# Optimization experiments

Measured on AMD Instinct MI355X. Metric: run time of the kernel, lower is better.

The kernel has to match this reference:

```python
import jax, jax.numpy as jnp
import numpy as np

L, H, P = 32768, 256, 256
DT_MIN, DT_MAX = 0.001, 0.1


def setup_inputs() -> dict:
    key = jax.random.key(0)
    ks = jax.random.split(key, 7)
    signal = jax.random.normal(ks[0], (L, H), jnp.float32)
    # stable HiPPO-like init: negative real part, random imaginary part
    lam_re = -(0.1 + 0.4 * jax.random.uniform(ks[1], (P,), jnp.float32))
    lam_im = jax.random.normal(ks[2], (P,), jnp.float32)
    Lambda_ri = jnp.stack([lam_re, lam_im], axis=-1)            # (P, 2)
    B_ri = jax.random.normal(ks[3], (P, H, 2), jnp.float32) / np.float32(np.sqrt(H))
    C_ri = jax.random.normal(ks[4], (H, P, 2), jnp.float32) / np.float32(np.sqrt(P))
    D = jax.random.uniform(ks[5], (H,), jnp.float32)
    log_step = jnp.log(DT_MIN + (DT_MAX - DT_MIN) * jax.random.uniform(ks[6], (P,), jnp.float32))
    return {"signal": signal, "Lambda_ri": Lambda_ri, "B_ri": B_ri,
            "C_ri": C_ri, "D": D, "log_step": log_step}


def reference(signal, Lambda_ri, B_ri, C_ri, D, log_step):
    # --- get_BC_tilde (bcInit='dense'): B stored real (P,H,2) -> complex ---
    Lambda = jax.lax.complex(Lambda_ri[..., 0], Lambda_ri[..., 1])   # (P,)
    B_tilde = jax.lax.complex(B_ri[..., 0], B_ri[..., 1])            # (P, H)
    C_tilde = jax.lax.complex(C_ri[..., 0], C_ri[..., 1])            # (H, P)

    # --- discretize_zoh ---
    step = jnp.exp(log_step)                                          # (P,) step_scale = 1.0
    Lambda_bar = jnp.exp(Lambda * step)                               # (P,) complex
    B_bar = ((Lambda_bar - 1.0) / Lambda)[:, None] * B_tilde          # (P, H) complex

    # --- apply_ssm: Bu_elements = vmap(u -> B_bar @ u) over time ---
    Bu = signal.astype(Lambda_bar.dtype) @ B_bar.T                    # (L, P) complex
    Lam = jnp.broadcast_to(Lambda_bar, Bu.shape)                      # (L, P)

    def binop(qi, qj):
        A_i, Bu_i = qi
        A_j, Bu_j = qj
        return (A_j * A_i, Bu_j + A_j * Bu_i)

    _, xs = jax.lax.associative_scan(binop, (Lam, Bu), axis=0)        # (L, P)

    # y = Re(C_tilde @ x) + D * u, vectorized over time
    y = jnp.real(xs @ C_tilde.T) + D * signal                         # (L, H)
    return y
```

## Files before the change

### kernel.cpp

```cpp
#include <hip/hip_runtime.h>
#include <math.h>

constexpr int L = 32768;
constexpr int H = 256;
constexpr int P = 256;
constexpr int T = 64;
constexpr int NC = L / T;
constexpr int N1 = 2 * P;
constexpr int LDA = 40;
constexpr int LDEP = 130;

typedef __attribute__((ext_vector_type(8))) short short8;
typedef __attribute__((ext_vector_type(4))) float f32x4;

__device__ __forceinline__ unsigned f2bf(float f) {
  unsigned u = __float_as_uint(f);
  return (u + 0x7FFFu + ((u >> 16) & 1u)) >> 16;
}
__device__ __forceinline__ float bf_lo(unsigned u) { return __uint_as_float(u << 16); }
__device__ __forceinline__ float bf_hi(unsigned u) { return __uint_as_float(u & 0xFFFF0000u); }

__device__ __forceinline__ void gload_lds16(const unsigned short* g, unsigned short* l) {
  __builtin_amdgcn_global_load_lds(
      (const __attribute__((address_space(1))) unsigned int*)(g),
      (__attribute__((address_space(3))) unsigned int*)(l), 16, 0, 0);
}

#define KBAR(N) do { \
    asm volatile("s_waitcnt vmcnt(" #N ") lgkmcnt(0)" ::: "memory"); \
    __builtin_amdgcn_s_barrier(); \
    __builtin_amdgcn_sched_barrier(0); \
  } while (0)

#define VMEM_FENCE() __builtin_amdgcn_sched_barrier(0x38F)

__device__ __forceinline__ void lambda_bar_of(const float* __restrict__ lam,
                                              const float* __restrict__ lstep,
                                              int p, float& lbr, float& lbi) {
  float lr = lam[2 * p], li = lam[2 * p + 1];
  float st = expf(lstep[p]);
  float ea = expf(lr * st);
  lbr = ea * cosf(li * st);
  lbi = ea * sinf(li * st);
}

__global__ __launch_bounds__(256) void k_prep(const float* __restrict__ lam,
                                              const float* __restrict__ lstep,
                                              const float* __restrict__ Bri,
                                              const float* __restrict__ Cri,
                                              unsigned short* __restrict__ Bcat,
                                              unsigned short* __restrict__ Ccat,
                                              float* __restrict__ powr,
                                              float* __restrict__ powi) {
  int idx = blockIdx.x * 256 + threadIdx.x;
  if (idx < N1 * H) {
    int n = idx >> 8, k = idx & 255;
    int p = n >> 1, comp = n & 1;
    float lr = lam[2 * p], li = lam[2 * p + 1];
    float st = expf(lstep[p]);
    float ea = expf(lr * st);
    float lbr = ea * cosf(li * st), lbi = ea * sinf(li * st);
    float inv = 1.0f / (lr * lr + li * li);
    float nr = lbr - 1.0f;
    float fr = (nr * lr + lbi * li) * inv;
    float fi = (lbi * lr - nr * li) * inv;
    float br = Bri[2 * (p * H + k)], bi = Bri[2 * (p * H + k) + 1];
    float v = (comp == 0) ? (fr * br - fi * bi) : (fr * bi + fi * br);
    Bcat[idx] = (unsigned short)f2bf(v);
  } else if (idx < 2 * N1 * H) {
    int j = idx - N1 * H;
    int h = j >> 9, k2 = j & 511;
    int p = k2 >> 1;
    float v = ((k2 & 1) == 0) ? Cri[2 * (h * P + p)] : -Cri[2 * (h * P + p) + 1];
    Ccat[j] = (unsigned short)f2bf(v);
  } else {
    int r = idx - 2 * N1 * H;
    int t = r >> 8, p = r & 255;
    float lr = lam[2 * p], li = lam[2 * p + 1];
    float st = expf(lstep[p]);
    float e = (float)(t + 1);
    float er = expf(e * lr * st);
    powr[r] = er * cosf(e * li * st);
    powi[r] = er * sinf(e * li * st);
  }
}

__global__ __launch_bounds__(256, 3) void k_gemm1s(const float* __restrict__ sig,
                                                   const unsigned short* __restrict__ Bcat,
                                                   const float* __restrict__ lam,
                                                   const float* __restrict__ lstep,
                                                   unsigned short* __restrict__ Xl,
                                                   float* __restrict__ Sr,
                                                   float* __restrict__ Si) {
  constexpr int K = 256, NIT = K / 32;
  __shared__ __align__(16) char smem[53248];
  unsigned short* sA[2] = {(unsigned short*)smem, (unsigned short*)smem + 5120};
  unsigned short* sB[4] = {(unsigned short*)(smem + 20480), (unsigned short*)(smem + 28672),
                           (unsigned short*)(smem + 36864), (unsigned short*)(smem + 45056)};
  float* sEpi = (float*)smem;
  const int tid = threadIdx.x;
  const int lane = tid & 63;
  const int wave = tid >> 6;
  const int wr = (wave >> 1) * 64, wc = (wave & 1) * 64;
  const int m0 = blockIdx.x * 128, n0 = blockIdx.y * 128;
  const int ar = tid >> 1, aq = (tid & 1) * 16;
  const int brow = ((tid >> 6) << 4) | (tid & 15);
  const int bko = ((tid >> 4) & 3) * 8;
  const int frow = lane & 15, fk = (lane >> 4) * 8;
  const int hb = (wave & 1) * 2048;
  f32x4 acc[4][4];
#pragma unroll
  for (int i = 0; i < 4; i++)
#pragma unroll
    for (int j = 0; j < 4; j++) acc[i][j] = (f32x4){0.f, 0.f, 0.f, 0.f};

  float4 aR0[4], aR1[4];
  const float* abase = sig + (size_t)(m0 + ar) * K + aq;
#define LOAD_A(R, k0) { const float* s_ = abase + (k0); \
    R[0] = *(const float4*)(s_); R[1] = *(const float4*)(s_ + 4); \
    R[2] = *(const float4*)(s_ + 8); R[3] = *(const float4*)(s_ + 12); }
#define WRITE_A(R, dst) { uint4 w0, w1; \
    w0.x = f2bf(R[0].x) | (f2bf(R[0].y) << 16); w0.y = f2bf(R[0].z) | (f2bf(R[0].w) << 16); \
    w0.z = f2bf(R[1].x) | (f2bf(R[1].y) << 16); w0.w = f2bf(R[1].z) | (f2bf(R[1].w) << 16); \
    w1.x = f2bf(R[2].x) | (f2bf(R[2].y) << 16); w1.y = f2bf(R[2].z) | (f2bf(R[2].w) << 16); \
    w1.z = f2bf(R[3].x) | (f2bf(R[3].y) << 16); w1.w = f2bf(R[3].z) | (f2bf(R[3].w) << 16); \
    *(uint4*)((dst) + ar * LDA + aq) = w0; *(uint4*)((dst) + ar * LDA + aq + 8) = w1; }
#define ISSUE_B(k0, buf) { \
    gload_lds16(Bcat + (size_t)(n0 + brow) * K + (k0) + bko, sB[buf] + tid * 8); \
    gload_lds16(Bcat + (size_t)(n0 + 64 + brow) * K + (k0) + bko, sB[buf] + 2048 + tid * 8); }

  LOAD_A(aR0, 0);
  LOAD_A(aR1, 32);
  VMEM_FENCE();
  ISSUE_B(0, 0);
  ISSUE_B(32, 1);
  ISSUE_B(64, 2);
  VMEM_FENCE();
  WRITE_A(aR0, sA[0]);
  LOAD_A(aR0, 64);
  VMEM_FENCE();
  KBAR(8);
#pragma unroll
  for (int it = 0; it < NIT; it++) {
    if (it + 1 < NIT) {
      if (((it + 1) & 1) == 0) { WRITE_A(aR0, sA[0]); } else { WRITE_A(aR1, sA[1]); }
    }
    VMEM_FENCE();
    if (it + 3 < NIT) {
      if (((it + 3) & 1) == 0) { LOAD_A(aR0, (it + 3) * 32); } else { LOAD_A(aR1, (it + 3) * 32); }
    }
    VMEM_FENCE();
    if (it + 3 < NIT) ISSUE_B((it + 3) * 32, (it + 3) & 3);
    VMEM_FENCE();
    short8 af[4], bfr[4];
#pragma unroll
    for (int i = 0; i < 4; i++) af[i] = *(const short8*)(sA[it & 1] + (wr + i * 16 + frow) * LDA + fk);
#pragma unroll
    for (int j = 0; j < 4; j++) bfr[j] = *(const short8*)(sB[it & 3] + hb + (j * 64 + lane) * 8);
#pragma unroll
    for (int i = 0; i < 4; i++)
#pragma unroll
      for (int j = 0; j < 4; j++)
        acc[i][j] = __builtin_amdgcn_mfma_f32_16x16x32_bf16(af[i], bfr[j], acc[i][j], 0, 0, 0);
    if (it + 1 < NIT) {
      if (it < NIT - 3) { KBAR(12); }
      else if (it == NIT - 3) { KBAR(6); }
      else { KBAR(0); }
    }
  }
  __syncthreads();

  const int crow = (lane >> 4) * 4, ccol = wc + (lane & 15);
#pragma unroll
  for (int half = 0; half < 2; half++) {
    if ((wave >> 1) == half) {
#pragma unroll
      for (int i = 0; i < 4; i++)
#pragma unroll
        for (int j = 0; j < 4; j++)
#pragma unroll
          for (int g = 0; g < 4; g++)
            sEpi[(crow + i * 16 + g) * LDEP + ccol + j * 16] = acc[i][j][g];
    }
    __syncthreads();
    if (tid < 64) {
      const int pl = tid;
      const int gp = (n0 >> 1) + pl;
      const int c = blockIdx.x * 2 + half;
      float lbr, lbi;
      lambda_bar_of(lam, lstep, gp, lbr, lbi);
      float xr = 0.f, xi = 0.f;
      const float* e = sEpi + 2 * pl;
      const size_t gbase = (size_t)(m0 + half * 64) * N1 + n0 + 2 * pl;
      for (int tb = 0; tb < T; tb += 8) {
        float2 v[8];
#pragma unroll
        for (int u = 0; u < 8; u++) v[u] = *(const float2*)(e + (tb + u) * LDEP);
        unsigned ov[8];
#pragma unroll
        for (int u = 0; u < 8; u++) {
          float nr = fmaf(lbr, xr, fmaf(-lbi, xi, v[u].x));
          float ni = fmaf(lbr, xi, fmaf(lbi, xr, v[u].y));
          xr = nr; xi = ni;
          ov[u] = f2bf(xr) | (f2bf(xi) << 16);
        }
#pragma unroll
        for (int u = 0; u < 8; u++)
          *(unsigned*)(Xl + gbase + (size_t)(tb + u) * N1) = ov[u];
      }
      Sr[(size_t)gp * NC + c] = xr;
      Si[(size_t)gp * NC + c] = xi;
    }
    __syncthreads();
  }
#undef LOAD_A
#undef WRITE_A
#undef ISSUE_B
}

__global__ __launch_bounds__(64) void k_carry2(const float* __restrict__ lam,
                                               const float* __restrict__ lstep,
                                               const float* __restrict__ Sr,
                                               const float* __restrict__ Si,
                                               float* __restrict__ car, float* __restrict__ cai) {
  const int p = blockIdx.x;
  const int t = threadIdx.x;
  float lr = lam[2 * p], li = lam[2 * p + 1];
  float st = expf(lstep[p]);
  float eT = expf((float)T * lr * st);
  float lTr = eT * cosf((float)T * li * st);
  float lTi = eT * sinf((float)T * li * st);
  float vr[8], vi[8];
  {
    const float* srp = Sr + (size_t)p * NC + t * 8;
    const float* sip = Si + (size_t)p * NC + t * 8;
    float4 a0 = *(const float4*)(srp), a1 = *(const float4*)(srp + 4);
    float4 b0 = *(const float4*)(sip), b1 = *(const float4*)(sip + 4);
    vr[0] = a0.x; vr[1] = a0.y; vr[2] = a0.z; vr[3] = a0.w;
    vr[4] = a1.x; vr[5] = a1.y; vr[6] = a1.z; vr[7] = a1.w;
    vi[0] = b0.x; vi[1] = b0.y; vi[2] = b0.z; vi[3] = b0.w;
    vi[4] = b1.x; vi[5] = b1.y; vi[6] = b1.z; vi[7] = b1.w;
  }
  float Br = 0.f, Bi = 0.f;
#pragma unroll
  for (int u = 0; u < 8; u++) {
    float nr = fmaf(lTr, Br, fmaf(-lTi, Bi, vr[u]));
    float ni = fmaf(lTr, Bi, fmaf(lTi, Br, vi[u]));
    Br = nr; Bi = ni;
  }
  float e8 = expf(8.0f * (float)T * lr * st);
  float Ar = e8 * cosf(8.0f * (float)T * li * st);
  float Ai = e8 * sinf(8.0f * (float)T * li * st);
#pragma unroll
  for (int d = 1; d < 64; d <<= 1) {
    float Aor = __shfl_up(Ar, d), Aoi = __shfl_up(Ai, d);
    float Bor = __shfl_up(Br, d), Boi = __shfl_up(Bi, d);
    if (t >= d) {
      float nBr = Ar * Bor - Ai * Boi + Br;
      float nBi = Ar * Boi + Ai * Bor + Bi;
      float nAr = Aor * Ar - Aoi * Ai;
      float nAi = Aor * Ai + Aoi * Ar;
      Br = nBr; Bi = nBi; Ar = nAr; Ai = nAi;
    }
  }
  float cr = __shfl_up(Br, 1), ci = __shfl_up(Bi, 1);
  if (t == 0) { cr = 0.f; ci = 0.f; }
#pragma unroll
  for (int u = 0; u < 8; u++) {
    car[(t * 8 + u) * P + p] = cr;
    cai[(t * 8 + u) * P + p] = ci;
    float nr = fmaf(lTr, cr, fmaf(-lTi, ci, vr[u]));
    float ni = fmaf(lTr, ci, fmaf(lTi, cr, vi[u]));
    cr = nr; ci = ni;
  }
}

__global__ __launch_bounds__(256, 3) void k_gemm2f(const unsigned short* __restrict__ Xl,
                                                   const unsigned short* __restrict__ Ccat,
                                                   const float* __restrict__ powr,
                                                   const float* __restrict__ powi,
                                                   const float* __restrict__ car,
                                                   const float* __restrict__ cai,
                                                   const float* __restrict__ sig,
                                                   const float* __restrict__ Dv,
                                                   float* __restrict__ out) {
  constexpr int K = 512, NIT = K / 32;
  __shared__ __align__(16) char smem[53248];
  unsigned short* sA[2] = {(unsigned short*)smem, (unsigned short*)smem + 5120};
  unsigned short* sB[4] = {(unsigned short*)(smem + 20480), (unsigned short*)(smem + 28672),
                           (unsigned short*)(smem + 36864), (unsigned short*)(smem + 45056)};
  const int tid = threadIdx.x;
  const int lane = tid & 63;
  const int wave = tid >> 6;
  const int wr = (wave >> 1) * 64, wc = (wave & 1) * 64;
  const int m0 = blockIdx.x * 128, n0 = blockIdx.y * 128;
  const int ar = tid >> 1, aq = (tid & 1) * 16;
  const int t_ = ar & 63;
  const int cc = blockIdx.x * 2 + (ar >> 6);
  const int brow = ((tid >> 6) << 4) | (tid & 15);
  const int bko = ((tid >> 4) & 3) * 8;
  const int frow = lane & 15, fk = (lane >> 4) * 8;
  const int hb = (wave & 1) * 2048;
  f32x4 acc[4][4];
#pragma unroll
  for (int i = 0; i < 4; i++)
#pragma unroll
    for (int j = 0; j < 4; j++) acc[i][j] = (f32x4){0.f, 0.f, 0.f, 0.f};

  uint4 x0a, x1a, x0b, x1b;
  float4 pra0, pra1, pia0, pia1, cra0, cra1, cia0, cia1;
  float4 prb0, prb1, pib0, pib1, crb0, crb1, cib0, cib1;
  const unsigned short* xbase = Xl + (size_t)(m0 + ar) * N1 + aq;
  const float* prb = powr + t_ * P;
  const float* pib = powi + t_ * P;
  const float* crb = car + cc * P;
  const float* cib = cai + cc * P;
#define LOAD_X(A0, A1, k0) { \
    A0 = *(const uint4*)(xbase + (k0)); A1 = *(const uint4*)(xbase + (k0) + 8); }
#define LOAD_PC(PR0, PR1, PI0, PI1, CR0, CR1, CI0, CI1, k0) { \
    const int p0_ = ((k0) >> 1) + (tid & 1) * 8; \
    PR0 = *(const float4*)(prb + p0_); PR1 = *(const float4*)(prb + p0_ + 4); \
    PI0 = *(const float4*)(pib + p0_); PI1 = *(const float4*)(pib + p0_ + 4); \
    CR0 = *(const float4*)(crb + p0_); CR1 = *(const float4*)(crb + p0_ + 4); \
    CI0 = *(const float4*)(cib + p0_); CI1 = *(const float4*)(cib + p0_ + 4); }
#define WRITE_A2(XA, XB, PR0, PR1, PI0, PI1, CR0, CR1, CI0, CI1, dst) { \
    unsigned xw[8] = {XA.x, XA.y, XA.z, XA.w, XB.x, XB.y, XB.z, XB.w}; \
    float pr_[8] = {PR0.x, PR0.y, PR0.z, PR0.w, PR1.x, PR1.y, PR1.z, PR1.w}; \
    float pi_[8] = {PI0.x, PI0.y, PI0.z, PI0.w, PI1.x, PI1.y, PI1.z, PI1.w}; \
    float cr_[8] = {CR0.x, CR0.y, CR0.z, CR0.w, CR1.x, CR1.y, CR1.z, CR1.w}; \
    float ci_[8] = {CI0.x, CI0.y, CI0.z, CI0.w, CI1.x, CI1.y, CI1.z, CI1.w}; \
    unsigned wo[8]; \
    _Pragma("unroll") for (int j_ = 0; j_ < 8; j_++) { \
      float xgr = bf_lo(xw[j_]) + (pr_[j_] * cr_[j_] - pi_[j_] * ci_[j_]); \
      float xgi = bf_hi(xw[j_]) + (pr_[j_] * ci_[j_] + pi_[j_] * cr_[j_]); \
      wo[j_] = f2bf(xgr) | (f2bf(xgi) << 16); } \
    uint4 w0, w1; \
    w0.x = wo[0]; w0.y = wo[1]; w0.z = wo[2]; w0.w = wo[3]; \
    w1.x = wo[4]; w1.y = wo[5]; w1.z = wo[6]; w1.w = wo[7]; \
    *(uint4*)((dst) + ar * LDA + aq) = w0; *(uint4*)((dst) + ar * LDA + aq + 8) = w1; }
#define ISSUE_B2(k0, buf) { \
    gload_lds16(Ccat + (size_t)(n0 + brow) * K + (k0) + bko, sB[buf] + tid * 8); \
    gload_lds16(Ccat + (size_t)(n0 + 64 + brow) * K + (k0) + bko, sB[buf] + 2048 + tid * 8); }

  LOAD_X(x0a, x1a, 0);
  LOAD_PC(pra0, pra1, pia0, pia1, cra0, cra1, cia0, cia1, 0);
  LOAD_X(x0b, x1b, 32);
  LOAD_PC(prb0, prb1, pib0, pib1, crb0, crb1, cib0, cib1, 32);
  VMEM_FENCE();
  ISSUE_B2(0, 0);
  ISSUE_B2(32, 1);
  ISSUE_B2(64, 2);
  VMEM_FENCE();
  WRITE_A2(x0a, x1a, pra0, pra1, pia0, pia1, cra0, cra1, cia0, cia1, sA[0]);
  LOAD_X(x0a, x1a, 64);
  LOAD_PC(pra0, pra1, pia0, pia1, cra0, cra1, cia0, cia1, 64);
  VMEM_FENCE();
  KBAR(14);
#pragma unroll
  for (int it = 0; it < NIT; it++) {
    if (it + 1 < NIT) {
      if (((it + 1) & 1) == 0) {
        WRITE_A2(x0a, x1a, pra0, pra1, pia0, pia1, cra0, cra1, cia0, cia1, sA[0]);
      } else {
        WRITE_A2(x0b, x1b, prb0, prb1, pib0, pib1, crb0, crb1, cib0, cib1, sA[1]);
      }
    }
    VMEM_FENCE();
    if (it + 3 < NIT) {
      if (((it + 3) & 1) == 0) {
        LOAD_X(x0a, x1a, (it + 3) * 32);
        LOAD_PC(pra0, pra1, pia0, pia1, cra0, cra1, cia0, cia1, (it + 3) * 32);
      } else {
        LOAD_X(x0b, x1b, (it + 3) * 32);
        LOAD_PC(prb0, prb1, pib0, pib1, crb0, crb1, cib0, cib1, (it + 3) * 32);
      }
    }
    VMEM_FENCE();
    if (it + 3 < NIT) ISSUE_B2((it + 3) * 32, (it + 3) & 3);
    VMEM_FENCE();
    short8 af[4], bfr[4];
#pragma unroll
    for (int i = 0; i < 4; i++) af[i] = *(const short8*)(sA[it & 1] + (wr + i * 16 + frow) * LDA + fk);
#pragma unroll
    for (int j = 0; j < 4; j++) bfr[j] = *(const short8*)(sB[it & 3] + hb + (j * 64 + lane) * 8);
#pragma unroll
    for (int i = 0; i < 4; i++)
#pragma unroll
      for (int j = 0; j < 4; j++)
        acc[i][j] = __builtin_amdgcn_mfma_f32_16x16x32_bf16(af[i], bfr[j], acc[i][j], 0, 0, 0);
    if (it + 1 < NIT) {
      if (it < NIT - 3) { KBAR(24); }
      else if (it == NIT - 3) { KBAR(12); }
      else { KBAR(0); }
    }
  }

  const int crow = wr + (lane >> 4) * 4, ccol = wc + (lane & 15);
  float dcol[4];
#pragma unroll
  for (int j = 0; j < 4; j++) dcol[j] = Dv[n0 + ccol + j * 16];
#pragma unroll
  for (int i = 0; i < 4; i++)
#pragma unroll
    for (int j = 0; j < 4; j++) {
      int col = n0 + ccol + j * 16;
#pragma unroll
      for (int g = 0; g < 4; g++) {
        int row = m0 + crow + i * 16 + g;
        out[(size_t)row * H + col] = acc[i][j][g] + dcol[j] * sig[(size_t)row * H + col];
      }
    }
#undef LOAD_X
#undef LOAD_PC
#undef WRITE_A2
#undef ISSUE_B2
}

extern "C" void kernel_launch(void* const* d_in, const int* in_sizes, int n_in,
                              void* d_out, int out_size, void* d_ws, size_t ws_size,
                              hipStream_t stream) {
  const float* sig = (const float*)d_in[0];
  const float* lam = (const float*)d_in[1];
  const float* Bri = (const float*)d_in[2];
  const float* Cri = (const float*)d_in[3];
  const float* Dv  = (const float*)d_in[4];
  const float* lst = (const float*)d_in[5];
  float* out = (float*)d_out;

  unsigned short* Bcat = (unsigned short*)d_ws;
  unsigned short* Ccat = Bcat + (size_t)N1 * H;
  unsigned short* Xl   = Ccat + (size_t)H * N1;
  float* powr = (float*)(Xl + (size_t)L * N1);
  float* powi = powr + T * P;
  float* Sr   = powi + T * P;
  float* Si   = Sr + NC * P;
  float* car  = Si + NC * P;
  float* cai  = car + NC * P;

  k_prep<<<(2 * N1 * H + T * P) / 256, 256, 0, stream>>>(lam, lst, Bri, Cri,
                                                         Bcat, Ccat, powr, powi);
  dim3 g1(L / 128, N1 / 128);
  k_gemm1s<<<g1, 256, 0, stream>>>(sig, Bcat, lam, lst, Xl, Sr, Si);
  k_carry2<<<NC / 2, 64, 0, stream>>>(lam, lst, Sr, Si, car, cai);
  dim3 g2(L / 128, H / 128);
  k_gemm2f<<<g2, 256, 0, stream>>>(Xl, Ccat, powr, powi, car, cai, sig, Dv, out);
}
```

Baseline: 161.1 us.

## Pre-convert signal to bf16 fragment layout in prep, DMA A tiles directly to LDS

The prep kernel now also converts the fp32 signal into a bf16 buffer laid out in MFMA fragment order per 128-row panel and 32-wide k-step. The first GEMM then loads A tiles with direct global-to-LDS loads instead of loading fp32 into registers and converting in the main loop. Buffering changes to three A stages and two B stages, shared memory shrinks, and the occupancy hint rises to 4 blocks. In exchange the signal conversion adds an extra global pass and a 16 MB workspace write and read in a separate kernel.

New measurement: 152.4 us. 1.06x faster.

```diff
diff --git a/kernel.cpp b/kernel.cpp
--- a/kernel.cpp
+++ b/kernel.cpp
@@ -44,14 +44,16 @@
   lbi = ea * sinf(li * st);
 }
 
-__global__ __launch_bounds__(256) void k_prep(const float* __restrict__ lam,
+__global__ __launch_bounds__(256) void k_prep(const float* __restrict__ sig,
+                                              const float* __restrict__ lam,
                                               const float* __restrict__ lstep,
                                               const float* __restrict__ Bri,
                                               const float* __restrict__ Cri,
                                               unsigned short* __restrict__ Bcat,
                                               unsigned short* __restrict__ Ccat,
                                               float* __restrict__ powr,
-                                              float* __restrict__ powi) {
+                                              float* __restrict__ powi,
+                                              unsigned short* __restrict__ sigt) {
   int idx = blockIdx.x * 256 + threadIdx.x;
   if (idx < N1 * H) {
     int n = idx >> 8, k = idx & 255;
@@ -73,7 +75,7 @@
     int p = k2 >> 1;
     float v = ((k2 & 1) == 0) ? Cri[2 * (h * P + p)] : -Cri[2 * (h * P + p) + 1];
     Ccat[j] = (unsigned short)f2bf(v);
-  } else {
+  } else if (idx < 2 * N1 * H + T * P) {
     int r = idx - 2 * N1 * H;
     int t = r >> 8, p = r & 255;
     float lr = lam[2 * p], li = lam[2 * p + 1];
@@ -82,90 +84,88 @@
     float er = expf(e * lr * st);
     powr[r] = er * cosf(e * li * st);
     powi[r] = er * sinf(e * li * st);
-  }
-}
-
-__global__ __launch_bounds__(256, 3) void k_gemm1s(const float* __restrict__ sig,
+  } else {
+    int C = idx - (2 * N1 * H + T * P);
+    int panel = C >> 12;
+    int ks = (C >> 9) & 7;
+    int c = C & 511;
+    int row = ((c >> 8) << 6) + (((c >> 6) & 3) << 4) + (c & 15);
+    int kk = ((c >> 4) & 3) << 3;
+    const float* s = sig + (size_t)(panel * 128 + row) * 256 + ks * 32 + kk;
+    float4 a = *(const float4*)(s);
+    float4 b = *(const float4*)(s + 4);
+    uint4 w;
+    w.x = f2bf(a.x) | (f2bf(a.y) << 16);
+    w.y = f2bf(a.z) | (f2bf(a.w) << 16);
+    w.z = f2bf(b.x) | (f2bf(b.y) << 16);
+    w.w = f2bf(b.z) | (f2bf(b.w) << 16);
+    *(uint4*)(sigt + (size_t)C * 8) = w;
+  }
+}
+
+__global__ __launch_bounds__(256, 4) void k_gemm1s(const unsigned short* __restrict__ sigt,
                                                    const unsigned short* __restrict__ Bcat,
                                                    const float* __restrict__ lam,
                                                    const float* __restrict__ lstep,
                                                    unsigned short* __restrict__ Xl,
                                                    float* __restrict__ Sr,
                                                    float* __restrict__ Si) {
-  constexpr int K = 256, NIT = K / 32;
-  __shared__ __align__(16) char smem[53248];
-  unsigned short* sA[2] = {(unsigned short*)smem, (unsigned short*)smem + 5120};
-  unsigned short* sB[4] = {(unsigned short*)(smem + 20480), (unsigned short*)(smem + 28672),
-                           (unsigned short*)(smem + 36864), (unsigned short*)(smem + 45056)};
+  constexpr int NIT = 8;
+  __shared__ __align__(16) char smem[40960];
+  unsigned short* sA[3] = {(unsigned short*)smem, (unsigned short*)(smem + 8192),
+                           (unsigned short*)(smem + 16384)};
+  unsigned short* sB[2] = {(unsigned short*)(smem + 24576), (unsigned short*)(smem + 32768)};
   float* sEpi = (float*)smem;
   const int tid = threadIdx.x;
   const int lane = tid & 63;
   const int wave = tid >> 6;
-  const int wr = (wave >> 1) * 64, wc = (wave & 1) * 64;
+  const int wc = (wave & 1) * 64;
   const int m0 = blockIdx.x * 128, n0 = blockIdx.y * 128;
-  const int ar = tid >> 1, aq = (tid & 1) * 16;
   const int brow = ((tid >> 6) << 4) | (tid & 15);
   const int bko = ((tid >> 4) & 3) * 8;
-  const int frow = lane & 15, fk = (lane >> 4) * 8;
   const int hb = (wave & 1) * 2048;
+  const int afb = (wave >> 1) * 256;
+  const unsigned short* apan = sigt + (size_t)blockIdx.x * 32768;
   f32x4 acc[4][4];
 #pragma unroll
   for (int i = 0; i < 4; i++)
 #pragma unroll
     for (int j = 0; j < 4; j++) acc[i][j] = (f32x4){0.f, 0.f, 0.f, 0.f};
 
-  float4 aR0[4], aR1[4];
-  const float* abase = sig + (size_t)(m0 + ar) * K + aq;
-#define LOAD_A(R, k0) { const float* s_ = abase + (k0); \
-    R[0] = *(const float4*)(s_); R[1] = *(const float4*)(s_ + 4); \
-    R[2] = *(const float4*)(s_ + 8); R[3] = *(const float4*)(s_ + 12); }
-#define WRITE_A(R, dst) { uint4 w0, w1; \
-    w0.x = f2bf(R[0].x) | (f2bf(R[0].y) << 16); w0.y = f2bf(R[0].z) | (f2bf(R[0].w) << 16); \
-    w0.z = f2bf(R[1].x) | (f2bf(R[1].y) << 16); w0.w = f2bf(R[1].z) | (f2bf(R[1].w) << 16); \
-    w1.x = f2bf(R[2].x) | (f2bf(R[2].y) << 16); w1.y = f2bf(R[2].z) | (f2bf(R[2].w) << 16); \
-    w1.z = f2bf(R[3].x) | (f2bf(R[3].y) << 16); w1.w = f2bf(R[3].z) | (f2bf(R[3].w) << 16); \
-    *(uint4*)((dst) + ar * LDA + aq) = w0; *(uint4*)((dst) + ar * LDA + aq + 8) = w1; }
-#define ISSUE_B(k0, buf) { \
-    gload_lds16(Bcat + (size_t)(n0 + brow) * K + (k0) + bko, sB[buf] + tid * 8); \
-    gload_lds16(Bcat + (size_t)(n0 + 64 + brow) * K + (k0) + bko, sB[buf] + 2048 + tid * 8); }
-
-  LOAD_A(aR0, 0);
-  LOAD_A(aR1, 32);
-  VMEM_FENCE();
-  ISSUE_B(0, 0);
-  ISSUE_B(32, 1);
-  ISSUE_B(64, 2);
-  VMEM_FENCE();
-  WRITE_A(aR0, sA[0]);
-  LOAD_A(aR0, 64);
-  VMEM_FENCE();
-  KBAR(8);
+#define ISSUE_A1(ks, buf) { \
+    gload_lds16(apan + (ks) * 4096 + tid * 8, sA[buf] + tid * 8); \
+    gload_lds16(apan + (ks) * 4096 + 2048 + tid * 8, sA[buf] + 2048 + tid * 8); }
+#define ISSUE_B1(ks, buf) { \
+    gload_lds16(Bcat + (size_t)(n0 + brow) * 256 + (ks) * 32 + bko, sB[buf] + tid * 8); \
+    gload_lds16(Bcat + (size_t)(n0 + 64 + brow) * 256 + (ks) * 32 + bko, sB[buf] + 2048 + tid * 8); }
+
+  ISSUE_A1(0, 0);
+  VMEM_FENCE();
+  ISSUE_B1(0, 0);
+  VMEM_FENCE();
+  ISSUE_A1(1, 1);
+  VMEM_FENCE();
+  KBAR(2);
 #pragma unroll
   for (int it = 0; it < NIT; it++) {
-    if (it + 1 < NIT) {
-      if (((it + 1) & 1) == 0) { WRITE_A(aR0, sA[0]); } else { WRITE_A(aR1, sA[1]); }
-    }
+    if (it + 1 < NIT) ISSUE_B1(it + 1, (it + 1) & 1);
     VMEM_FENCE();
-    if (it + 3 < NIT) {
-      if (((it + 3) & 1) == 0) { LOAD_A(aR0, (it + 3) * 32); } else { LOAD_A(aR1, (it + 3) * 32); }
-    }
+    if (it + 2 < NIT) ISSUE_A1(it + 2, (it + 2) % 3);
     VMEM_FENCE();
-    if (it + 3 < NIT) ISSUE_B((it + 3) * 32, (it + 3) & 3);
-    VMEM_FENCE();
+    const unsigned short* sAc = sA[it % 3];
+    const unsigned short* sBc = sB[it & 1];
     short8 af[4], bfr[4];
 #pragma unroll
-    for (int i = 0; i < 4; i++) af[i] = *(const short8*)(sA[it & 1] + (wr + i * 16 + frow) * LDA + fk);
-#pragma unroll
-    for (int j = 0; j < 4; j++) bfr[j] = *(const short8*)(sB[it & 3] + hb + (j * 64 + lane) * 8);
+    for (int i = 0; i < 4; i++) af[i] = *(const short8*)(sAc + (afb + i * 64 + lane) * 8);
+#pragma unroll
+    for (int j = 0; j < 4; j++) bfr[j] = *(const short8*)(sBc + hb + (j * 64 + lane) * 8);
 #pragma unroll
     for (int i = 0; i < 4; i++)
 #pragma unroll
       for (int j = 0; j < 4; j++)
         acc[i][j] = __builtin_amdgcn_mfma_f32_16x16x32_bf16(af[i], bfr[j], acc[i][j], 0, 0, 0);
     if (it + 1 < NIT) {
-      if (it < NIT - 3) { KBAR(12); }
-      else if (it == NIT - 3) { KBAR(6); }
-      else { KBAR(0); }
+      if (it + 2 < NIT) { KBAR(2); } else { KBAR(0); }
     }
   }
   __syncthreads();
@@ -213,9 +213,8 @@
     }
     __syncthreads();
   }
-#undef LOAD_A
-#undef WRITE_A
-#undef ISSUE_B
+#undef ISSUE_A1
+#undef ISSUE_B1
 }
 
 __global__ __launch_bounds__(64) void k_carry2(const float* __restrict__ lam,
@@ -436,11 +435,12 @@
   float* Si   = Sr + NC * P;
   float* car  = Si + NC * P;
   float* cai  = car + NC * P;
-
-  k_prep<<<(2 * N1 * H + T * P) / 256, 256, 0, stream>>>(lam, lst, Bri, Cri,
-                                                         Bcat, Ccat, powr, powi);
+  unsigned short* sigt = (unsigned short*)(cai + NC * P);
+
+  k_prep<<<(2 * N1 * H + T * P + L * H / 8) / 256, 256, 0, stream>>>(
+      sig, lam, lst, Bri, Cri, Bcat, Ccat, powr, powi, sigt);
   dim3 g1(L / 128, N1 / 128);
-  k_gemm1s<<<g1, 256, 0, stream>>>(sig, Bcat, lam, lst, Xl, Sr, Si);
+  k_gemm1s<<<g1, 256, 0, stream>>>(sigt, Bcat, lam, lst, Xl, Sr, Si);
   k_carry2<<<NC / 2, 64, 0, stream>>>(lam, lst, Sr, Si, car, cai);
   dim3 g2(L / 128, H / 128);
   k_gemm2f<<<g2, 256, 0, stream>>>(Xl, Ccat, powr, powi, car, cai, sig, Dv, out);
```
